# Optimization experiments

Hardware: AMD Instinct MI355X
Metric: run time of the kernel (lower is better)

The kernel has to match this reference:

```python
import jax, jax.numpy as jnp
import numpy as np

TOKENS, IN_F, OUT_F = 16, 4096, 11008


def setup_inputs() -> dict:
    key = jax.random.key(0)
    k1, k2, k3, k4 = jax.random.split(key, 4)
    x = jax.random.normal(k1, (TOKENS, IN_F), dtype=jnp.float32)
    weight_int8 = jax.random.randint(k2, (OUT_F, IN_F), 0, 127, dtype=jnp.int32)
    # per-row scale, clamped >= 1e-8 as in the torch module
    scale = jnp.maximum(jax.random.uniform(k3, (OUT_F, 1), dtype=jnp.float32) * 0.02, 1e-8)
    bias = jax.random.normal(k4, (OUT_F,), dtype=jnp.float32)
    return {"x": x, "weight_int8": weight_int8, "scale": scale, "bias": bias}


def reference(x, weight_int8, scale, bias):
    # dequantize: [out, in] fp32 weight, cast to activation dtype
    w = (weight_int8.astype(jnp.float32) * scale).astype(x.dtype)
    # F.linear: x @ w.T + bias
    return jnp.einsum('ti,oi->to', x, w) + bias.astype(x.dtype)
```

## Files before the change

kernel.cpp:

```cpp
#include <hip/hip_runtime.h>
#include <hip/hip_bf16.h>

typedef float f32x4 __attribute__((ext_vector_type(4)));
typedef short short8 __attribute__((ext_vector_type(8)));

constexpr int TOKENS = 16;
constexpr int IN_F   = 4096;
constexpr int OUT_F  = 11008;
constexpr int WAVES  = 8;
constexpr int SEG_K  = IN_F / WAVES;
constexpr int NTILES = OUT_F / 16;

__device__ __forceinline__ unsigned short bf16_rne(float f) {
    unsigned u = __builtin_bit_cast(unsigned, f);
    u += 0x7fffu + ((u >> 16) & 1u);
    return (unsigned short)(u >> 16);
}
__device__ __forceinline__ short bf16_from_int(int v) {
    float f = (float)v;
    return (short)(__builtin_bit_cast(unsigned, f) >> 16);
}

__global__ __launch_bounds__(256) void cvt_x_kernel(
    const float* __restrict__ x, unsigned short* __restrict__ xb)
{
    const int i = (blockIdx.x * 256 + threadIdx.x) * 4;
    float4 v = *(const float4*)(x + i);
    ushort4 o;
    o.x = bf16_rne(v.x); o.y = bf16_rne(v.y);
    o.z = bf16_rne(v.z); o.w = bf16_rne(v.w);
    *(ushort4*)(xb + i) = o;
}

__global__ __launch_bounds__(512, 2) void Int8Linear_kernel(
    const unsigned short* __restrict__ xb,
    const int*   __restrict__ w,
    const float* __restrict__ scale,
    const float* __restrict__ bias,
    float*       __restrict__ out)
{
    const int tid  = threadIdx.x;
    const int wave = tid >> 6;
    const int lane = tid & 63;
    const int m    = lane & 15;
    const int g    = lane >> 4;
    const int n0   = blockIdx.x * 16;

    const unsigned short* xp = xb + (size_t)m * IN_F + wave * SEG_K + g * 8;
    const int*            wp = w  + (size_t)(n0 + m) * IN_F + wave * SEG_K + g * 8;

    f32x4 acc = {0.f, 0.f, 0.f, 0.f};

    #pragma unroll 8
    for (int kb = 0; kb < SEG_K / 32; ++kb) {
        short8 a  = *(const short8*)xp;
        int4   wa = *(const int4*)wp;
        int4   wb = *(const int4*)(wp + 4);
        xp += 32; wp += 32;

        short8 b;
        b[0] = bf16_from_int(wa.x); b[1] = bf16_from_int(wa.y);
        b[2] = bf16_from_int(wa.z); b[3] = bf16_from_int(wa.w);
        b[4] = bf16_from_int(wb.x); b[5] = bf16_from_int(wb.y);
        b[6] = bf16_from_int(wb.z); b[7] = bf16_from_int(wb.w);

        acc = __builtin_amdgcn_mfma_f32_16x16x32_bf16(a, b, acc, 0, 0, 0);
    }

    __shared__ float red[WAVES][16][16];
    #pragma unroll
    for (int r = 0; r < 4; ++r)
        red[wave][g * 4 + r][m] = acc[r];
    __syncthreads();

    if (tid < 256) {
        const int row = tid >> 4;
        const int col = tid & 15;
        float s = 0.f;
        #pragma unroll
        for (int v = 0; v < WAVES; ++v)
            s += red[v][row][col];
        const int o = n0 + col;
        out[(size_t)row * OUT_F + o] = s * scale[o] + bias[o];
    }
}

extern "C" void kernel_launch(void* const* d_in, const int* in_sizes, int n_in,
                              void* d_out, int out_size, void* d_ws, size_t ws_size,
                              hipStream_t stream) {
    const float* x     = (const float*)d_in[0];
    const int*   w     = (const int*)d_in[1];
    const float* scale = (const float*)d_in[2];
    const float* bias  = (const float*)d_in[3];
    float*       out   = (float*)d_out;
    unsigned short* xb = (unsigned short*)d_ws;

    cvt_x_kernel<<<64, 256, 0, stream>>>(x, xb);
    Int8Linear_kernel<<<NTILES, 512, 0, stream>>>(xb, w, scale, bias, out);
}
```

Before: 44.60 us.

## Stream weight chunks into LDS via async global_load_lds with double buffering

The kernel now streams the int32 weight tile in 256-wide K chunks straight into padded LDS using global_load_lds, double-buffered so the next chunk loads while the current one is consumed. Each block drops from 8 to 4 waves, and each wave handles two 32-wide K slices per chunk instead of a fixed K segment. The aim is better memory-level parallelism and overlap on this bandwidth-bound weight stream. In exchange it adds a block barrier per chunk (16 chunks) and uses about 33 KB of LDS per block, which may limit occupancy.

```diff
diff --git a/kernel.cpp b/kernel.cpp
--- a/kernel.cpp
+++ b/kernel.cpp
@@ -4,12 +4,16 @@
 typedef float f32x4 __attribute__((ext_vector_type(4)));
 typedef short short8 __attribute__((ext_vector_type(8)));
 
-constexpr int TOKENS = 16;
-constexpr int IN_F   = 4096;
-constexpr int OUT_F  = 11008;
-constexpr int WAVES  = 8;
-constexpr int SEG_K  = IN_F / WAVES;
-constexpr int NTILES = OUT_F / 16;
+constexpr int IN_F    = 4096;
+constexpr int OUT_F   = 11008;
+constexpr int NTILES  = OUT_F / 16;
+constexpr int CHUNK_K = 256;
+constexpr int NCHUNK  = IN_F / CHUNK_K;
+constexpr int ROWW    = 260;
+constexpr int WAVES   = 4;
+
+#define GLBP(p) ((const __attribute__((address_space(1))) void*)(p))
+#define LDSP(p) ((__attribute__((address_space(3))) void*)(p))
 
 __device__ __forceinline__ unsigned short bf16_rne(float f) {
     unsigned u = __builtin_bit_cast(unsigned, f);
@@ -32,13 +36,15 @@
     *(ushort4*)(xb + i) = o;
 }
 
-__global__ __launch_bounds__(512, 2) void Int8Linear_kernel(
+__global__ __launch_bounds__(256, 4) void Int8Linear_kernel(
     const unsigned short* __restrict__ xb,
     const int*   __restrict__ w,
     const float* __restrict__ scale,
     const float* __restrict__ bias,
     float*       __restrict__ out)
 {
+    __shared__ uint32_t lds[2 * 16 * ROWW];
+
     const int tid  = threadIdx.x;
     const int wave = tid >> 6;
     const int lane = tid & 63;
@@ -46,43 +52,63 @@
     const int g    = lane >> 4;
     const int n0   = blockIdx.x * 16;
 
-    const unsigned short* xp = xb + (size_t)m * IN_F + wave * SEG_K + g * 8;
-    const int*            wp = w  + (size_t)(n0 + m) * IN_F + wave * SEG_K + g * 8;
+    auto stage = [&](int c) {
+        const int buf = (c & 1) * 16 * ROWW;
+        #pragma unroll
+        for (int r = 0; r < 4; ++r) {
+            const int row = wave * 4 + r;
+            const int* gp = w + (size_t)(n0 + row) * IN_F + c * CHUNK_K + lane * 4;
+            uint32_t*  lp = (uint32_t*)&lds[buf + row * ROWW + lane * 4];
+            __builtin_amdgcn_global_load_lds(
+                (const __attribute__((address_space(1))) uint32_t*)gp,
+                (__attribute__((address_space(3))) uint32_t*)lp, 16, 0, 0);
+        }
+    };
 
     f32x4 acc = {0.f, 0.f, 0.f, 0.f};
+    stage(0);
 
-    #pragma unroll 8
-    for (int kb = 0; kb < SEG_K / 32; ++kb) {
-        short8 a  = *(const short8*)xp;
-        int4   wa = *(const int4*)wp;
-        int4   wb = *(const int4*)(wp + 4);
-        xp += 32; wp += 32;
+    for (int c = 0; c < NCHUNK; ++c) {
+        __syncthreads();
+        if (c + 1 < NCHUNK) stage(c + 1);
 
-        short8 b;
-        b[0] = bf16_from_int(wa.x); b[1] = bf16_from_int(wa.y);
-        b[2] = bf16_from_int(wa.z); b[3] = bf16_from_int(wa.w);
-        b[4] = bf16_from_int(wb.x); b[5] = bf16_from_int(wb.y);
-        b[6] = bf16_from_int(wb.z); b[7] = bf16_from_int(wb.w);
+        const int buf = (c & 1) * 16 * ROWW;
+        #pragma unroll
+        for (int s = 0; s < 2; ++s) {
+            const int kc = (wave * 2 + s) * 32;
+            const int k0 = c * CHUNK_K + kc;
 
-        acc = __builtin_amdgcn_mfma_f32_16x16x32_bf16(a, b, acc, 0, 0, 0);
+            short8 a = *(const short8*)(xb + (size_t)m * IN_F + k0 + g * 8);
+
+            const uint32_t* bw = &lds[buf + m * ROWW + kc + g * 8];
+            int4 wa = *(const int4*)bw;
+            int4 wb = *(const int4*)(bw + 4);
+
+            short8 b;
+            b[0] = bf16_from_int(wa.x); b[1] = bf16_from_int(wa.y);
+            b[2] = bf16_from_int(wa.z); b[3] = bf16_from_int(wa.w);
+            b[4] = bf16_from_int(wb.x); b[5] = bf16_from_int(wb.y);
+            b[6] = bf16_from_int(wb.z); b[7] = bf16_from_int(wb.w);
+
+            acc = __builtin_amdgcn_mfma_f32_16x16x32_bf16(a, b, acc, 0, 0, 0);
+        }
     }
 
-    __shared__ float red[WAVES][16][16];
+    __syncthreads();
+    float* red = (float*)lds;
     #pragma unroll
     for (int r = 0; r < 4; ++r)
-        red[wave][g * 4 + r][m] = acc[r];
+        red[(wave * 16 + g * 4 + r) * 16 + m] = acc[r];
     __syncthreads();
 
-    if (tid < 256) {
-        const int row = tid >> 4;
-        const int col = tid & 15;
-        float s = 0.f;
-        #pragma unroll
-        for (int v = 0; v < WAVES; ++v)
-            s += red[v][row][col];
-        const int o = n0 + col;
-        out[(size_t)row * OUT_F + o] = s * scale[o] + bias[o];
-    }
+    const int row = tid >> 4;
+    const int col = tid & 15;
+    float s = 0.f;
+    #pragma unroll
+    for (int v = 0; v < WAVES; ++v)
+        s += red[(v * 16 + row) * 16 + col];
+    const int o = n0 + col;
+    out[(size_t)row * OUT_F + o] = s * scale[o] + bias[o];
 }
 
 extern "C" void kernel_launch(void* const* d_in, const int* in_sizes, int n_in,
@@ -96,5 +122,5 @@
     unsigned short* xb = (unsigned short*)d_ws;
 
     cvt_x_kernel<<<64, 256, 0, stream>>>(x, xb);
-    Int8Linear_kernel<<<NTILES, 512, 0, stream>>>(xb, w, scale, bias, out);
+    Int8Linear_kernel<<<NTILES, 256, 0, stream>>>(xb, w, scale, bias, out);
 }
```

Measured after the change: 45.58 us. 1.02x slower.
